# Performance work log

Measured on AMD Instinct MI355X. Metric: run time of the kernel, lower is better.

Reference implementation:

```python
import jax, jax.numpy as jnp
import numpy as np


def _hilbert_filter(S):
    # scipy.signal.hilbert analytic-signal spectrum multiplier
    h = np.zeros(S, dtype=np.float32)
    h[0] = 1.0
    if S % 2 == 0:
        h[S // 2] = 1.0
        h[1:S // 2] = 2.0
    else:
        h[1:(S + 1) // 2] = 2.0
    return h


def setup_inputs() -> dict:
    key = jax.random.key(0)
    B, C, S = 16, 64, 2048
    x = jax.random.normal(key, (B, C, S), dtype=jnp.float32)
    return {"x": x}


def reference(x) -> jnp.ndarray:
    B, C, S = x.shape
    h = jnp.asarray(_hilbert_filter(S))
    # Analytic signal via FFT (batched over all B*C channels at once,
    # instead of recomputing hilbert() per (i,j) pair as the torch loop does)
    analytic = jnp.fft.ifft(jnp.fft.fft(x, axis=-1) * h, axis=-1)  # [B,C,S] complex
    theta = jnp.angle(analytic)                                    # [B,C,S]
    # Pairwise instantaneous phase differences: [B,C,C,S]
    d = theta[:, :, None, :] - theta[:, None, :, :]
    # angle(exp(1j*d)) wraps d to (-pi,pi]; original zeroes exact +/-pi values.
    # sign(sin(d)) == sign(wrapped d) with +/-pi (and 0) mapped to 0 -- identical math.
    pli = jnp.abs(jnp.mean(jnp.sign(jnp.sin(d)), axis=-1))         # [B,C,C]
    # diagonal: d == 0 -> sign 0 -> mean 0, matching the skipped i==j entries
    return pli.astype(jnp.float32)
```

## Files before the change

kernel.cpp:

```cpp
#include <hip/hip_runtime.h>

#define Bv 16
#define Cv 64
#define Sv 2048
#define NSEG 32
#define SSEG 64
#define ROWS 68
#define NTILE 144
#define MAGICF 0x4F1BBCDCu

__device__ __forceinline__ void bf_f(float2& u, float2& v, const float2 w) {
    const float dr = u.x - v.x, di = u.y - v.y;
    u.x += v.x; u.y += v.y;
    v.x = dr * w.x - di * w.y;
    v.y = dr * w.y + di * w.x;
}
__device__ __forceinline__ void bf_i(float2& u, float2& v, const float2 w) {
    const float vr = v.x * w.x + v.y * w.y;
    const float vi = v.y * w.x - v.x * w.y;
    v.x = u.x - vr; v.y = u.y - vi;
    u.x += vr; u.y += vi;
}
__device__ __forceinline__ float2 csq(const float2 a) {
    return make_float2(a.x * a.x - a.y * a.y, 2.0f * a.x * a.y);
}
__device__ __forceinline__ float2 cm1(const float2 a) {
    const float cq = 0.70710678118654752f;
    return make_float2(cq * (a.x + a.y), cq * (a.y - a.x));
}
__device__ __forceinline__ float2 cmi(const float2 a) {
    return make_float2(a.y, -a.x);
}
__device__ __forceinline__ int pad(int n) { return n + (n >> 3); }

__device__ __forceinline__ unsigned int pang(const float x, const float h) {
    const float p = h * __builtin_amdgcn_rcpf(fabsf(x) + fabsf(h));
    const int i = (int)(p * 1073741824.0f);
    return (x >= 0.0f) ? (unsigned int)i : 0x80000000u - (unsigned int)i;
}

__device__ __forceinline__ void st_agent(unsigned int* p, unsigned int v) {
    __hip_atomic_store(p, v, __ATOMIC_RELAXED, __HIP_MEMORY_SCOPE_AGENT);
}
__device__ __forceinline__ unsigned int ld_agent(const unsigned int* p) {
    return __hip_atomic_load((unsigned int*)p, __ATOMIC_RELAXED, __HIP_MEMORY_SCOPE_AGENT);
}
__device__ __forceinline__ void wait_batch(const unsigned int* f, int t) {
    if (t < 32) {
        int guard = 0;
        while (ld_agent(&f[t]) != MAGICF && guard < (1 << 20)) {
            ++guard;
            __builtin_amdgcn_s_sleep(2);
        }
    }
    __syncthreads();
}

__global__ __launch_bounds__(256, 2) void pli_one(const float* __restrict__ x,
                                                  unsigned int* __restrict__ u,
                                                  unsigned int* __restrict__ part,
                                                  unsigned int* __restrict__ flags1,
                                                  unsigned int* __restrict__ flags2,
                                                  float* __restrict__ out) {
    __shared__ __align__(16) unsigned char shraw[(Sv + Sv / 8) * sizeof(float2)];
    float2* const zz = (float2*)shraw;
    unsigned int* const uL = (unsigned int*)shraw;
    const int t = threadIdx.x;
    const int blk = blockIdx.x;
    const int b = blk >> 5;
    const int g = blk & (NSEG - 1);

    {
        const int c0 = blk * 2;
        const float* x0 = x + (size_t)c0 * Sv;
        const float* x1 = x0 + Sv;

        const float PI = 3.14159265358979323846f;
        float2 bA4, bB4, bC2;
        sincosf(-PI * (float)t * (1.0f / 1024.0f), &bA4.y, &bA4.x);
        sincosf(-PI * (float)(t & 31) * (1.0f / 128.0f), &bB4.y, &bB4.x);
        sincosf(-PI * (float)(t & 7) * (1.0f / 16.0f), &bC2.y, &bC2.x);
        const float2 bA2 = csq(bA4), bA1 = csq(bA2);
        const float2 bB2 = csq(bB4), bB1 = csq(bB2);
        const float2 bC1 = csq(bC2);

        float xa[8], xb[8];
        float2 z[8];
        #pragma unroll
        for (int k = 0; k < 8; ++k) {
            xa[k] = x0[t + 256 * k];
            xb[k] = x1[t + 256 * k];
            z[k] = make_float2(xa[k], xb[k]);
        }

        {
            const float2 w1 = cm1(bA4);
            bf_f(z[0], z[4], bA4);      bf_f(z[1], z[5], w1);
            bf_f(z[2], z[6], cmi(bA4)); bf_f(z[3], z[7], cmi(w1));
            const float2 wB = cmi(bA2);
            bf_f(z[0], z[2], bA2); bf_f(z[1], z[3], wB);
            bf_f(z[4], z[6], bA2); bf_f(z[5], z[7], wB);
            bf_f(z[0], z[1], bA1); bf_f(z[2], z[3], bA1);
            bf_f(z[4], z[5], bA1); bf_f(z[6], z[7], bA1);
        }
        #pragma unroll
        for (int k = 0; k < 8; ++k) zz[pad(t + 256 * k)] = z[k];
        __syncthreads();

        {
            const int r = t & 31, base = (t >> 5) * 256 + r;
            #pragma unroll
            for (int k = 0; k < 8; ++k) z[k] = zz[pad(base + 32 * k)];
            const float2 w1 = cm1(bB4);
            bf_f(z[0], z[4], bB4);      bf_f(z[1], z[5], w1);
            bf_f(z[2], z[6], cmi(bB4)); bf_f(z[3], z[7], cmi(w1));
            const float2 wB = cmi(bB2);
            bf_f(z[0], z[2], bB2); bf_f(z[1], z[3], wB);
            bf_f(z[4], z[6], bB2); bf_f(z[5], z[7], wB);
            bf_f(z[0], z[1], bB1); bf_f(z[2], z[3], bB1);
            bf_f(z[4], z[5], bB1); bf_f(z[6], z[7], bB1);
            #pragma unroll
            for (int k = 0; k < 8; ++k) zz[pad(base + 32 * k)] = z[k];
        }
        __syncthreads();

        {
            const int r = t & 7, base0 = (t >> 3) * 32 + r, base1 = base0 + 1024;
            #pragma unroll
            for (int k = 0; k < 4; ++k) {
                z[k] = zz[pad(base0 + 8 * k)];
                z[4 + k] = zz[pad(base1 + 8 * k)];
            }
            const float2 wB = cmi(bC2);
            bf_f(z[0], z[2], bC2); bf_f(z[1], z[3], wB);
            bf_f(z[4], z[6], bC2); bf_f(z[5], z[7], wB);
            bf_f(z[0], z[1], bC1); bf_f(z[2], z[3], bC1);
            bf_f(z[4], z[5], bC1); bf_f(z[6], z[7], bC1);
            #pragma unroll
            for (int k = 0; k < 4; ++k) {
                zz[pad(base0 + 8 * k)] = z[k];
                zz[pad(base1 + 8 * k)] = z[4 + k];
            }
        }
        __syncthreads();

        {
            const int base = 8 * t;
            #pragma unroll
            for (int k = 0; k < 8; ++k) z[k] = zz[pad(base + k)];
            const float cq = 0.70710678118654752f;
            const float2 W1  = make_float2(1.0f, 0.0f);
            const float2 W41 = make_float2(cq, -cq);
            const float2 W42 = make_float2(0.0f, -1.0f);
            const float2 W43 = make_float2(-cq, -cq);
            bf_f(z[0], z[4], W1);  bf_f(z[1], z[5], W41);
            bf_f(z[2], z[6], W42); bf_f(z[3], z[7], W43);
            bf_f(z[0], z[2], W1); bf_f(z[1], z[3], W42);
            bf_f(z[4], z[6], W1); bf_f(z[5], z[7], W42);
            bf_f(z[0], z[1], W1); bf_f(z[2], z[3], W1);
            bf_f(z[4], z[5], W1); bf_f(z[6], z[7], W1);
            const float inv = 1.0f / (float)Sv;
            #pragma unroll
            for (int k = 0; k < 8; ++k) {
                const int kk = (int)(__brev((unsigned)(base + k)) >> 21);
                const float m = (kk == 0 || kk == Sv / 2) ? inv : (kk < Sv / 2 ? 2.0f * inv : 0.0f);
                z[k].x *= m; z[k].y *= m;
            }
            bf_i(z[0], z[1], W1); bf_i(z[2], z[3], W1);
            bf_i(z[4], z[5], W1); bf_i(z[6], z[7], W1);
            bf_i(z[0], z[2], W1); bf_i(z[1], z[3], W42);
            bf_i(z[4], z[6], W1); bf_i(z[5], z[7], W42);
            bf_i(z[0], z[4], W1);  bf_i(z[1], z[5], W41);
            bf_i(z[2], z[6], W42); bf_i(z[3], z[7], W43);
            #pragma unroll
            for (int k = 0; k < 8; ++k) zz[pad(base + k)] = z[k];
        }
        __syncthreads();

        {
            const int r = t & 7, base0 = (t >> 3) * 32 + r, base1 = base0 + 1024;
            #pragma unroll
            for (int k = 0; k < 4; ++k) {
                z[k] = zz[pad(base0 + 8 * k)];
                z[4 + k] = zz[pad(base1 + 8 * k)];
            }
            bf_i(z[0], z[1], bC1); bf_i(z[2], z[3], bC1);
            bf_i(z[4], z[5], bC1); bf_i(z[6], z[7], bC1);
            const float2 wB = cmi(bC2);
            bf_i(z[0], z[2], bC2); bf_i(z[1], z[3], wB);
            bf_i(z[4], z[6], bC2); bf_i(z[5], z[7], wB);
            #pragma unroll
            for (int k = 0; k < 4; ++k) {
                zz[pad(base0 + 8 * k)] = z[k];
                zz[pad(base1 + 8 * k)] = z[4 + k];
            }
        }
        __syncthreads();

        {
            const int r = t & 31, base = (t >> 5) * 256 + r;
            #pragma unroll
            for (int k = 0; k < 8; ++k) z[k] = zz[pad(base + 32 * k)];
            bf_i(z[0], z[1], bB1); bf_i(z[2], z[3], bB1);
            bf_i(z[4], z[5], bB1); bf_i(z[6], z[7], bB1);
            const float2 wB = cmi(bB2);
            bf_i(z[0], z[2], bB2); bf_i(z[1], z[3], wB);
            bf_i(z[4], z[6], bB2); bf_i(z[5], z[7], wB);
            const float2 w1 = cm1(bB4);
            bf_i(z[0], z[4], bB4);      bf_i(z[1], z[5], w1);
            bf_i(z[2], z[6], cmi(bB4)); bf_i(z[3], z[7], cmi(w1));
            #pragma unroll
            for (int k = 0; k < 8; ++k) zz[pad(base + 32 * k)] = z[k];
        }
        __syncthreads();

        {
            #pragma unroll
            for (int k = 0; k < 8; ++k) z[k] = zz[pad(t + 256 * k)];
            bf_i(z[0], z[1], bA1); bf_i(z[2], z[3], bA1);
            bf_i(z[4], z[5], bA1); bf_i(z[6], z[7], bA1);
            const float2 wB = cmi(bA2);
            bf_i(z[0], z[2], bA2); bf_i(z[1], z[3], wB);
            bf_i(z[4], z[6], bA2); bf_i(z[5], z[7], wB);
            const float2 w1 = cm1(bA4);
            bf_i(z[0], z[4], bA4);      bf_i(z[1], z[5], w1);
            bf_i(z[2], z[6], cmi(bA4)); bf_i(z[3], z[7], cmi(w1));
            unsigned int* u0 = u + (size_t)c0 * Sv;
            unsigned int* u1 = u0 + Sv;
            #pragma unroll
            for (int k = 0; k < 8; ++k) {
                const int n = t + 256 * k;
                const float ha = z[k].y - xb[k];
                const float hb = xa[k] - z[k].x;
                st_agent(&u0[n], pang(xa[k], ha));
                st_agent(&u1[n], pang(xb[k], hb));
            }
        }
    }

    __syncthreads();
    if (t == 0) st_agent(&flags1[blk], MAGICF);

    wait_batch(flags1 + b * 32, t);

    {
        const unsigned int* ub = u + (size_t)b * Cv * Sv + g * SSEG;

        unsigned int rstage[16];
        #pragma unroll
        for (int it = 0; it < 16; ++it) {
            const int e = t + 256 * it;
            rstage[it] = ld_agent(&ub[(size_t)(e >> 6) * Sv + (e & (SSEG - 1))]);
        }
        #pragma unroll
        for (int it = 0; it < 16; ++it) {
            const int e = t + 256 * it;
            uL[(e & (SSEG - 1)) * ROWS + (e >> 6)] = rstage[it];
        }
        __syncthreads();

        if (t < NTILE) {
            const int qi = t & 15;
            const int dq = t >> 4;
            const int i0 = qi * 4;
            const int j0 = ((qi + dq) & 15) * 4;
            int neg[4][4] = {};

            #pragma unroll 4
            for (int s = 0; s < SSEG; ++s) {
                const uint4 ui = *(const uint4*)&uL[s * ROWS + i0];
                const uint4 uj = *(const uint4*)&uL[s * ROWS + j0];
                const unsigned int uia[4] = {ui.x, ui.y, ui.z, ui.w};
                const unsigned int uja[4] = {uj.x, uj.y, uj.z, uj.w};
                #pragma unroll
                for (int a = 0; a < 4; ++a) {
                    #pragma unroll
                    for (int c = 0; c < 4; ++c) {
                        neg[a][c] += (int)((uia[a] - uja[c]) >> 31);
                    }
                }
            }

            unsigned int* Pb = part + ((size_t)blk * NTILE + t) * 4;
            #pragma unroll
            for (int a = 0; a < 4; ++a) {
                const unsigned int pk = (unsigned)neg[a][0] | ((unsigned)neg[a][1] << 8)
                                      | ((unsigned)neg[a][2] << 16) | ((unsigned)neg[a][3] << 24);
                st_agent(&Pb[a], pk);
            }
        }
    }

    __syncthreads();
    if (t == 0) st_agent(&flags2[blk], MAGICF);

    wait_batch(flags2 + b * 32, t);

    if (t < 128) {
        const unsigned int* pw = part + (size_t)b * (NSEG * NTILE * 4);
        const int ij = g * 128 + t;
        const int i = ij >> 6, j = ij & 63;
        const int qi = i >> 2, a = i & 3;
        const int qj = j >> 2, c = j & 3;
        const int gg = (qj - qi) & 15;
        int tile, wsel, bsel;
        if (gg <= 8) { tile = gg * 16 + qi;        wsel = a; bsel = c; }
        else         { tile = (16 - gg) * 16 + qj; wsel = c; bsel = a; }
        const unsigned int* pp = pw + tile * 4 + wsel;
        const int sh = 8 * bsel;
        int negsum = 0;
        #pragma unroll
        for (int s = 0; s < NSEG; ++s)
            negsum += (int)((ld_agent(&pp[s * (NTILE * 4)]) >> sh) & 255u);
        out[b * (Cv * Cv) + ij] = (i == j)
            ? 0.0f
            : fabsf((float)Sv - 2.0f * (float)negsum) * (1.0f / (float)Sv);
    }
}

extern "C" void kernel_launch(void* const* d_in, const int* in_sizes, int n_in,
                              void* d_out, int out_size, void* d_ws, size_t ws_size,
                              hipStream_t stream) {
    const float* x = (const float*)d_in[0];
    char* ws = (char*)d_ws;
    unsigned int* u      = (unsigned int*)ws;
    unsigned int* part   = (unsigned int*)(ws + (8u << 20));
    unsigned int* flags1 = (unsigned int*)(ws + (16u << 20));
    unsigned int* flags2 = (unsigned int*)(ws + (16u << 20) + 4096);
    float* out = (float*)d_out;

    hipLaunchKernelGGL(pli_one, dim3(Bv * Cv / 2), dim3(256), 0, stream,
                       x, u, part, flags1, flags2, out);
}
```

Measured before the change: 76.29 us.

## Stage phase and partial writes through LDS and use 64-bit agent-scope transfers

Phase codes are now written to LDS and then stored to global memory as coalesced 64-bit atomic stores. The cross-block gather reads 64-bit pairs, and partial counts are stored as two 64-bit words. The final reduction is reorganised per tile: each block loads its assigned tiles' partials into LDS, reduces them, and writes both symmetric output entries, so it no longer does strided 32-bit loads per output element. The aim is fewer, wider global memory transactions on the cross-block exchange, at the cost of extra LDS round-trips and barriers.

```diff
diff --git a/kernel.cpp b/kernel.cpp
--- a/kernel.cpp
+++ b/kernel.cpp
@@ -9,6 +9,8 @@
 #define NTILE 144
 #define MAGICF 0x4F1BBCDCu
 
+typedef unsigned long long u64t;
+
 __device__ __forceinline__ void bf_f(float2& u, float2& v, const float2 w) {
     const float dr = u.x - v.x, di = u.y - v.y;
     u.x += v.x; u.y += v.y;
@@ -44,6 +46,12 @@
 }
 __device__ __forceinline__ unsigned int ld_agent(const unsigned int* p) {
     return __hip_atomic_load((unsigned int*)p, __ATOMIC_RELAXED, __HIP_MEMORY_SCOPE_AGENT);
+}
+__device__ __forceinline__ void st_agent64(u64t* p, u64t v) {
+    __hip_atomic_store(p, v, __ATOMIC_RELAXED, __HIP_MEMORY_SCOPE_AGENT);
+}
+__device__ __forceinline__ u64t ld_agent64(const u64t* p) {
+    return __hip_atomic_load((u64t*)p, __ATOMIC_RELAXED, __HIP_MEMORY_SCOPE_AGENT);
 }
 __device__ __forceinline__ void wait_batch(const unsigned int* f, int t) {
     if (t < 32) {
@@ -225,15 +233,24 @@
             const float2 w1 = cm1(bA4);
             bf_i(z[0], z[4], bA4);      bf_i(z[1], z[5], w1);
             bf_i(z[2], z[6], cmi(bA4)); bf_i(z[3], z[7], cmi(w1));
-            unsigned int* u0 = u + (size_t)c0 * Sv;
-            unsigned int* u1 = u0 + Sv;
+
+            __syncthreads();
+            unsigned int* const uS = (unsigned int*)shraw;
             #pragma unroll
             for (int k = 0; k < 8; ++k) {
                 const int n = t + 256 * k;
                 const float ha = z[k].y - xb[k];
                 const float hb = xa[k] - z[k].x;
-                st_agent(&u0[n], pang(xa[k], ha));
-                st_agent(&u1[n], pang(xb[k], hb));
+                uS[n]        = pang(xa[k], ha);
+                uS[2048 + n] = pang(xb[k], hb);
+            }
+            __syncthreads();
+            const u64t* uS64 = (const u64t*)shraw;
+            u64t* ug = (u64t*)(u + (size_t)c0 * Sv);
+            #pragma unroll
+            for (int q = 0; q < 8; ++q) {
+                const int m = q * 256 + t;
+                st_agent64(&ug[m], uS64[m]);
             }
         }
     }
@@ -246,16 +263,21 @@
     {
         const unsigned int* ub = u + (size_t)b * Cv * Sv + g * SSEG;
 
-        unsigned int rstage[16];
+        u64t r64[8];
         #pragma unroll
-        for (int it = 0; it < 16; ++it) {
-            const int e = t + 256 * it;
-            rstage[it] = ld_agent(&ub[(size_t)(e >> 6) * Sv + (e & (SSEG - 1))]);
+        for (int p = 0; p < 8; ++p) {
+            const int idx = p * 256 + t;
+            const int ch = idx >> 5;
+            const int s2 = idx & 31;
+            r64[p] = ld_agent64((const u64t*)(ub + (size_t)ch * Sv) + s2);
         }
         #pragma unroll
-        for (int it = 0; it < 16; ++it) {
-            const int e = t + 256 * it;
-            uL[(e & (SSEG - 1)) * ROWS + (e >> 6)] = rstage[it];
+        for (int p = 0; p < 8; ++p) {
+            const int idx = p * 256 + t;
+            const int ch = idx >> 5;
+            const int s = (idx & 31) * 2;
+            uL[s * ROWS + ch] = (unsigned int)r64[p];
+            uL[(s + 1) * ROWS + ch] = (unsigned int)(r64[p] >> 32);
         }
         __syncthreads();
 
@@ -266,28 +288,34 @@
             const int j0 = ((qi + dq) & 15) * 4;
             int neg[4][4] = {};
 
-            #pragma unroll 4
-            for (int s = 0; s < SSEG; ++s) {
-                const uint4 ui = *(const uint4*)&uL[s * ROWS + i0];
-                const uint4 uj = *(const uint4*)&uL[s * ROWS + j0];
-                const unsigned int uia[4] = {ui.x, ui.y, ui.z, ui.w};
-                const unsigned int uja[4] = {uj.x, uj.y, uj.z, uj.w};
+            #pragma unroll 2
+            for (int s = 0; s < SSEG; s += 2) {
+                const uint4 ui0 = *(const uint4*)&uL[s * ROWS + i0];
+                const uint4 uj0 = *(const uint4*)&uL[s * ROWS + j0];
+                const uint4 ui1 = *(const uint4*)&uL[(s + 1) * ROWS + i0];
+                const uint4 uj1 = *(const uint4*)&uL[(s + 1) * ROWS + j0];
+                const unsigned int ia0[4] = {ui0.x, ui0.y, ui0.z, ui0.w};
+                const unsigned int ja0[4] = {uj0.x, uj0.y, uj0.z, uj0.w};
+                const unsigned int ia1[4] = {ui1.x, ui1.y, ui1.z, ui1.w};
+                const unsigned int ja1[4] = {uj1.x, uj1.y, uj1.z, uj1.w};
                 #pragma unroll
                 for (int a = 0; a < 4; ++a) {
                     #pragma unroll
                     for (int c = 0; c < 4; ++c) {
-                        neg[a][c] += (int)((uia[a] - uja[c]) >> 31);
+                        neg[a][c] += (int)(((ia0[a] - ja0[c]) >> 31)
+                                         + ((ia1[a] - ja1[c]) >> 31));
                     }
                 }
             }
 
-            unsigned int* Pb = part + ((size_t)blk * NTILE + t) * 4;
-            #pragma unroll
-            for (int a = 0; a < 4; ++a) {
-                const unsigned int pk = (unsigned)neg[a][0] | ((unsigned)neg[a][1] << 8)
-                                      | ((unsigned)neg[a][2] << 16) | ((unsigned)neg[a][3] << 24);
-                st_agent(&Pb[a], pk);
-            }
+            u64t* Pb = (u64t*)(part + ((size_t)blk * NTILE + t) * 4);
+            unsigned int pk[4];
+            #pragma unroll
+            for (int a = 0; a < 4; ++a)
+                pk[a] = (unsigned)neg[a][0] | ((unsigned)neg[a][1] << 8)
+                      | ((unsigned)neg[a][2] << 16) | ((unsigned)neg[a][3] << 24);
+            st_agent64(&Pb[0], (u64t)pk[0] | ((u64t)pk[1] << 32));
+            st_agent64(&Pb[1], (u64t)pk[2] | ((u64t)pk[3] << 32));
         }
     }
 
@@ -296,25 +324,41 @@
 
     wait_batch(flags2 + b * 32, t);
 
-    if (t < 128) {
-        const unsigned int* pw = part + (size_t)b * (NSEG * NTILE * 4);
-        const int ij = g * 128 + t;
-        const int i = ij >> 6, j = ij & 63;
-        const int qi = i >> 2, a = i & 3;
-        const int qj = j >> 2, c = j & 3;
-        const int gg = (qj - qi) & 15;
-        int tile, wsel, bsel;
-        if (gg <= 8) { tile = gg * 16 + qi;        wsel = a; bsel = c; }
-        else         { tile = (16 - gg) * 16 + qj; wsel = c; bsel = a; }
-        const unsigned int* pp = pw + tile * 4 + wsel;
-        const int sh = 8 * bsel;
-        int negsum = 0;
-        #pragma unroll
-        for (int s = 0; s < NSEG; ++s)
-            negsum += (int)((ld_agent(&pp[s * (NTILE * 4)]) >> sh) & 255u);
-        out[b * (Cv * Cv) + ij] = (i == j)
-            ? 0.0f
-            : fabsf((float)Sv - 2.0f * (float)negsum) * (1.0f / (float)Sv);
+    {
+        const int nt = (g < 16) ? 5 : 4;
+        u64t* const pT64 = (u64t*)shraw;
+        unsigned int* const pTu = (unsigned int*)shraw;
+
+        if (t < nt * 32) {
+            const int l = t >> 5, s = t & 31;
+            const int tau = g + 32 * l;
+            const u64t* src = (const u64t*)(part + ((size_t)(b * 32 + s) * NTILE + tau) * 4);
+            pT64[(l * 32 + s) * 2]     = ld_agent64(&src[0]);
+            pT64[(l * 32 + s) * 2 + 1] = ld_agent64(&src[1]);
+        }
+        __syncthreads();
+
+        if (t < nt * 16) {
+            const int l = t >> 4, slot = t & 15;
+            const int a = slot >> 2, c = slot & 3;
+            const unsigned int* row = pTu + (l * 32) * 4 + a;
+            const int sh = 8 * c;
+            int negsum = 0;
+            #pragma unroll 8
+            for (int s = 0; s < 32; ++s)
+                negsum += (int)((row[s * 4] >> sh) & 255u);
+
+            const int tau = g + 32 * l;
+            const int dq = tau >> 4, qi = tau & 15;
+            const int qj = (qi + dq) & 15;
+            const int i = qi * 4 + a, j = qj * 4 + c;
+            const float pli = (i == j)
+                ? 0.0f
+                : fabsf((float)Sv - 2.0f * (float)negsum) * (1.0f / (float)Sv);
+            float* ob = out + b * (Cv * Cv);
+            ob[i * 64 + j] = pli;
+            if (dq >= 1 && dq <= 7) ob[j * 64 + i] = pli;
+        }
     }
 }
 
```

Result: no change. 76.61 us (+0.4%).
